# Kernel tuning notes

Measured on AMD Instinct MI355X. Metric: run time of the kernel, lower is better.

## Reference

```python
import jax, jax.numpy as jnp
import numpy as np

B, S, D_MODEL = 2, 2048, 2048
N_HEADS, N_KV_HEADS, D_HEAD = 32, 8, 64
INIT_STD = 0.02


def setup_inputs() -> dict:
    key = jax.random.key(0)
    k1, k2, k3, k4, k5 = jax.random.split(key, 5)
    return {
        "residual": jax.random.normal(k1, (B, S, D_MODEL), dtype=jnp.float32),
        "W_Q": jax.random.normal(k2, (N_HEADS, D_HEAD, D_MODEL), dtype=jnp.float32) * INIT_STD,
        "W_K": jax.random.normal(k3, (N_KV_HEADS, D_HEAD, D_MODEL), dtype=jnp.float32) * INIT_STD,
        "W_V": jax.random.normal(k4, (N_KV_HEADS, D_HEAD, D_MODEL), dtype=jnp.float32) * INIT_STD,
        "W_O": jax.random.normal(k5, (N_HEADS, D_HEAD, D_MODEL), dtype=jnp.float32) * INIT_STD,
    }


def reference(residual, W_Q, W_K, W_V, W_O):
    # QKV projections: residual [b,p,d] x W [n,h,d] -> [b,p,n,h]
    q = jnp.einsum('bpd,nhd->bpnh', residual, W_Q)
    k = jnp.einsum('bpd,nhd->bpnh', residual, W_K)
    v = jnp.einsum('bpd,nhd->bpnh', residual, W_V)

    # GQA: repeat_interleave kv heads up to n_heads
    rep = N_HEADS // N_KV_HEADS
    k = jnp.repeat(k, rep, axis=2)  # [b, p, n_heads, h]
    v = jnp.repeat(v, rep, axis=2)

    # scaled dot-product scores: [b, n, q, k]
    scores = jnp.einsum('bqnh,bknh->bnqk', q, k) / jnp.sqrt(jnp.float32(D_HEAD))

    # causal mask (seq_len == total_len, no cache)
    seq_len = residual.shape[1]
    causal = jnp.tril(jnp.ones((seq_len, seq_len), dtype=bool))
    scores = jnp.where(causal[None, None, :, :], scores, jnp.float32(-jnp.inf))

    pattern = jax.nn.softmax(scores, axis=-1)

    # weighted sum of values: [b, q, n, h]
    attn_out = jnp.einsum('bnqk,bknh->bqnh', pattern, v)

    # output projection: [b, q, d_model]
    out = jnp.einsum('bqnh,nhd->bqd', attn_out, W_O)
    return out
```

## Files before the change

kernel.cpp:

```cpp
#include <hip/hip_runtime.h>


typedef __attribute__((ext_vector_type(8))) short short8;
typedef __attribute__((ext_vector_type(4))) short short4v;
typedef __attribute__((ext_vector_type(4))) float f32x4;

__device__ __forceinline__ short f2bs(float f) {
  unsigned u = __float_as_uint(f);
  u = (u + 0x7fffu + ((u >> 16) & 1u)) >> 16;
  return (short)u;
}
__device__ __forceinline__ float bs2f(short s) {
  return __uint_as_float(((unsigned)(unsigned short)s) << 16);
}

__device__ __forceinline__ void async_ld16(const void* g, void* l) {
  __builtin_amdgcn_global_load_lds((__attribute__((address_space(1))) void*)(g),
                                   (__attribute__((address_space(3))) void*)(l),
                                   16, 0, 0);
}

#define BARRIER()                       \
  do {                                  \
    asm volatile("" ::: "memory");      \
    __builtin_amdgcn_s_barrier();       \
    asm volatile("" ::: "memory");      \
  } while (0)
#define LGKM0()                                          \
  do {                                                   \
    asm volatile("s_waitcnt lgkmcnt(0)" ::: "memory");   \
    __builtin_amdgcn_sched_barrier(0);                   \
  } while (0)
#define VMCNT(n) asm volatile("s_waitcnt vmcnt(" #n ")" ::: "memory")
#define MFMA16(a, b, c) \
  (c) = __builtin_amdgcn_mfma_f32_16x16x32_bf16((a), (b), (c), 0, 0, 0)

__device__ __forceinline__ short4v pk4bf16(float p0, float p1, float p2,
                                           float p3) {
  union {
    unsigned u[2];
    short4v s;
  } pk;
  asm("v_cvt_pk_bf16_f32 %0, %1, %2" : "=v"(pk.u[0]) : "v"(p0), "v"(p1));
  asm("v_cvt_pk_bf16_f32 %0, %1, %2" : "=v"(pk.u[1]) : "v"(p2), "v"(p3));
  return pk.s;
}

__device__ __forceinline__ int block_sniff_f32(const short* __restrict__ r,
                                               int* bad) {
  if (threadIdx.x == 0) *bad = 0;
  __syncthreads();
  int my = 0;
  for (int i = threadIdx.x; i < 512; i += blockDim.x) {
    float x = bs2f(r[i]);
    if (!(fabsf(x) < 100.0f)) my = 1;
  }
  if (my) atomicOr(bad, 1);
  __syncthreads();
  return *bad;
}

__global__ __launch_bounds__(256) void prep_kernel(
    const void* __restrict__ s0, const void* __restrict__ s1,
    const void* __restrict__ s2, const void* __restrict__ s3,
    short* __restrict__ d0, short* __restrict__ d1, short* __restrict__ d2,
    short* __restrict__ d3, const void* __restrict__ wo,
    short* __restrict__ wot) {
  __shared__ short tile[64][65];
  __shared__ int badsh;
  const int isf = block_sniff_f32((const short*)s0, &badsh);
  const int bid = blockIdx.x;
  if (bid < 7168) {
    long off = (long)bid * 256 + threadIdx.x;
    const void* src;
    short* dst;
    if (off < 1048576) {
      src = s0; dst = d0;
    } else if ((off -= 1048576) < 524288) {
      src = s1; dst = d1;
    } else if ((off -= 524288) < 131072) {
      src = s2; dst = d2;
    } else {
      off -= 131072; src = s3; dst = d3;
    }
    const long e = off * 8;
    short8 v;
    if (isf) {
      const float* f = (const float*)src + e;
      const f32x4 a = *(const f32x4*)(f);
      const f32x4 b = *(const f32x4*)(f + 4);
#pragma unroll
      for (int j = 0; j < 4; ++j) {
        v[j] = f2bs(a[j]);
        v[4 + j] = f2bs(b[j]);
      }
    } else {
      v = *(const short8*)((const short*)src + e);
    }
    *(short8*)(dst + e) = v;
  } else {
    const int tb = bid - 7168;
    const int bx = tb & 31, by = tb >> 5;
    const int tx = threadIdx.x & 63, ty = threadIdx.x >> 6;
#pragma unroll
    for (int i = 0; i < 16; ++i) {
      const int r = ty + i * 4;
      const size_t idx = (size_t)(by * 64 + r) * 2048 + bx * 64 + tx;
      tile[r][tx] =
          isf ? f2bs(((const float*)wo)[idx]) : ((const short*)wo)[idx];
    }
    __syncthreads();
#pragma unroll
    for (int i = 0; i < 16; ++i) {
      const int r = ty + i * 4;
      wot[(size_t)(bx * 64 + r) * 2048 + by * 64 + tx] = tile[tx][r];
    }
  }
}

__device__ __forceinline__ void gemm256(const short* __restrict__ A, int lda,
                                        const short* __restrict__ B, int ldb,
                                        void* __restrict__ C, int ldc,
                                        int rowBase, int colBase, int K,
                                        short* SM, int outF32, float cscale) {
  const int t = threadIdx.x;
  const int wave = t >> 6;
  const int lane = t & 63;
  const int quad = lane >> 4;
  const int m16 = lane & 15;
  const int wr = (wave >> 2) * 128;
  const int wc = (wave & 3) * 64;

  short* const As0 = SM;
  short* const As1 = SM + 16384;
  short* const Bs0 = SM + 32768;
  short* const Bs1 = SM + 49152;

  const int sr = t >> 3;
  const int sc8 = ((t & 7) ^ (sr & 7)) * 8;
  const short* aS = A + (size_t)(rowBase + sr) * lda + sc8;
  const short* bS = B + (size_t)(colBase + sr) * ldb + sc8;
  const int dOff = wave * 512;

#define STG_A(buf, rg, kt) \
  async_ld16(aS + (size_t)(rg) * lda + (kt) * 64, (buf) + (rg) * 64 + dOff)
#define STG_B(buf, rg, kt) \
  async_ld16(bS + (size_t)(rg) * ldb + (kt) * 64, (buf) + (rg) * 64 + dOff)
#define RD(buf, row0, kh)                          \
  (*(const short8*)((buf) + ((row0) + m16) * 64 +  \
                    ((((kh) * 4 + quad) ^ (m16 & 7)) * 8)))

  const int nT = K >> 6;
  STG_A(As0, 0, 0); STG_A(As0, 64, 0); STG_A(As0, 128, 0); STG_A(As0, 192, 0);
  STG_B(Bs0, 0, 0); STG_B(Bs0, 64, 0); STG_B(Bs0, 128, 0); STG_B(Bs0, 192, 0);
  if (nT > 1) {
    STG_A(As1, 0, 1); STG_A(As1, 64, 1); STG_A(As1, 128, 1); STG_A(As1, 192, 1);
  }

  f32x4 acc[8][4] = {};
  for (int tt = 0; tt < nT; ++tt) {
    short* const Ac = (tt & 1) ? As1 : As0;
    short* const Bc = (tt & 1) ? Bs1 : Bs0;
    short* const Bn = (tt & 1) ? Bs0 : Bs1;

    if (tt + 1 < nT) {
      VMCNT(4);
    } else {
      VMCNT(0);
    }
    BARRIER();

    short8 alo[4][2], blo[2][2];
#pragma unroll
    for (int i = 0; i < 4; ++i) {
      alo[i][0] = RD(Ac, wr + i * 16, 0);
      alo[i][1] = RD(Ac, wr + i * 16, 1);
    }
#pragma unroll
    for (int j = 0; j < 2; ++j) {
      blo[j][0] = RD(Bc, wc + j * 16, 0);
      blo[j][1] = RD(Bc, wc + j * 16, 1);
    }
    if (tt + 1 < nT) { STG_B(Bn, 0, tt + 1); STG_B(Bn, 64, tt + 1); }
    BARRIER();
    LGKM0();
    __builtin_amdgcn_s_setprio(1);
#pragma unroll
    for (int i = 0; i < 4; ++i)
#pragma unroll
      for (int j = 0; j < 2; ++j) {
        MFMA16(alo[i][0], blo[j][0], acc[i][j]);
        MFMA16(alo[i][1], blo[j][1], acc[i][j]);
      }
    __builtin_amdgcn_s_setprio(0);
    BARRIER();

    short8 bhi[2][2];
#pragma unroll
    for (int j = 0; j < 2; ++j) {
      bhi[j][0] = RD(Bc, wc + 32 + j * 16, 0);
      bhi[j][1] = RD(Bc, wc + 32 + j * 16, 1);
    }
    if (tt + 1 < nT) { STG_B(Bn, 128, tt + 1); STG_B(Bn, 192, tt + 1); }
    BARRIER();
    LGKM0();
    __builtin_amdgcn_s_setprio(1);
#pragma unroll
    for (int i = 0; i < 4; ++i)
#pragma unroll
      for (int j = 0; j < 2; ++j) {
        MFMA16(alo[i][0], bhi[j][0], acc[i][2 + j]);
        MFMA16(alo[i][1], bhi[j][1], acc[i][2 + j]);
      }
    __builtin_amdgcn_s_setprio(0);
    BARRIER();

    short8 ahi[4][2];
#pragma unroll
    for (int i = 0; i < 4; ++i) {
      ahi[i][0] = RD(Ac, wr + 64 + i * 16, 0);
      ahi[i][1] = RD(Ac, wr + 64 + i * 16, 1);
    }
    BARRIER();
    if (tt + 2 < nT) { STG_A(Ac, 0, tt + 2); STG_A(Ac, 64, tt + 2); }
    LGKM0();
    __builtin_amdgcn_s_setprio(1);
#pragma unroll
    for (int i = 0; i < 4; ++i)
#pragma unroll
      for (int j = 0; j < 2; ++j) {
        MFMA16(ahi[i][0], blo[j][0], acc[4 + i][j]);
        MFMA16(ahi[i][1], blo[j][1], acc[4 + i][j]);
      }
    __builtin_amdgcn_s_setprio(0);
    BARRIER();

    if (tt + 2 < nT) { STG_A(Ac, 128, tt + 2); STG_A(Ac, 192, tt + 2); }
    __builtin_amdgcn_s_setprio(1);
#pragma unroll
    for (int i = 0; i < 4; ++i)
#pragma unroll
      for (int j = 0; j < 2; ++j) {
        MFMA16(ahi[i][0], bhi[j][0], acc[4 + i][2 + j]);
        MFMA16(ahi[i][1], bhi[j][1], acc[4 + i][2 + j]);
      }
    __builtin_amdgcn_s_setprio(0);
  }

  float* const F = (float*)SM + wave * 4096;
#pragma unroll
  for (int h = 0; h < 2; ++h) {
    if (h) LGKM0();
#pragma unroll
    for (int i = 0; i < 4; ++i)
#pragma unroll
      for (int j = 0; j < 4; ++j)
#pragma unroll
        for (int r = 0; r < 4; ++r)
          F[(i * 16 + quad * 4 + r) * 64 + j * 16 + m16] =
              acc[h * 4 + i][j][r] * cscale;
    LGKM0();
#pragma unroll
    for (int p = 0; p < 16; ++p) {
      const int row = p * 4 + quad;
      const f32x4 vv = *(const f32x4*)(F + row * 64 + m16 * 4);
      const size_t gi =
          (size_t)(rowBase + wr + h * 64 + row) * ldc + colBase + wc + m16 * 4;
      if (outF32) {
        *(f32x4*)((float*)C + gi) = vv;
      } else {
        short4v s;
#pragma unroll
        for (int r = 0; r < 4; ++r) s[r] = f2bs(vv[r]);
        *(short4v*)((short*)C + gi) = s;
      }
    }
  }
#undef STG_A
#undef STG_B
#undef RD
}

__global__ __launch_bounds__(512, 2) void qkv_gemm_kernel(
    const short* __restrict__ R, const short* __restrict__ WQ,
    const short* __restrict__ WK, const short* __restrict__ WV,
    short* __restrict__ q, short* __restrict__ k, short* __restrict__ v) {
  __shared__ __align__(16) short SM[65536];
  const int lid = blockIdx.x;
  const int nl = (lid & 7) * 24 + (lid >> 3);
  const int ct = nl % 12;
  const int rt = nl / 12;
  const short* Bm;
  short* Cout;
  int colBase, ldc;
  float cs = 1.0f;
  if (ct < 8) {
    Bm = WQ; Cout = q; colBase = ct * 256; ldc = 2048;
    cs = 0.125f * 1.44269504088896340736f;
  } else if (ct < 10) {
    Bm = WK; Cout = k; colBase = (ct - 8) * 256; ldc = 512;
  } else {
    Bm = WV; Cout = v; colBase = (ct - 10) * 256; ldc = 512;
  }
  gemm256(R, 2048, Bm, 2048, Cout, ldc, rt * 256, colBase, 2048, SM, 0, cs);
}

__global__ __launch_bounds__(512, 2) void out_gemm_kernel(
    const short* __restrict__ A, const short* __restrict__ Bt,
    void* __restrict__ C, const short* __restrict__ sniffsrc) {
  __shared__ __align__(16) short SM[65536];
  const int outF32 = block_sniff_f32(sniffsrc, (int*)SM);
  const int lid = blockIdx.x;
  const int nl = (lid & 7) * 16 + (lid >> 3);
  const int ct = nl & 7;
  const int rt = nl >> 3;
  gemm256(A, 2048, Bt, 2048, C, 2048, rt * 256, ct * 256, 2048, SM, outF32,
          1.0f);
}

__global__ __launch_bounds__(256) void vt_kernel(const short* __restrict__ v,
                                                 short* __restrict__ vt) {
  __shared__ short tile[64][65];
  const int hb = blockIdx.x * 64, pb = blockIdx.y * 64, b = blockIdx.z;
  const int tx = threadIdx.x & 63, ty = threadIdx.x >> 6;
#pragma unroll
  for (int i = 0; i < 16; ++i) {
    const int r = ty + i * 4;
    tile[r][tx] = v[((size_t)(b * 2048 + pb + r)) * 512 + hb + tx];
  }
  __syncthreads();
#pragma unroll
  for (int i = 0; i < 16; ++i) {
    const int r = ty + i * 4;
    vt[((size_t)(b * 512 + hb + r)) * 2048 + pb + tx] = tile[tx][r];
  }
}

__global__ __launch_bounds__(256, 3) void attn_kernel(
    const short* __restrict__ qbuf, const short* __restrict__ kbuf,
    const short* __restrict__ vtb, short* __restrict__ obuf) {
  __shared__ __align__(16) short Ks[2][64 * 64];
  __shared__ __align__(16) short Vs[2][64 * 64];
  __shared__ __align__(16) short Pb[4][32 * 64];

  const int b = blockIdx.x >> 3;
  const int kv = blockIdx.x & 7;
  const int qc = 63 - blockIdx.y;
  const int t = threadIdx.x;
  const int wave = t >> 6;
  const int hd = kv * 4 + wave;
  const int lane = t & 63;
  const int quad = lane >> 4;
  const int col = lane & 15;
  const int rb0 = qc * 32;

  short8 qf[2][2];
#pragma unroll
  for (int nt = 0; nt < 2; ++nt) {
    const int qr = rb0 + nt * 16 + col;
    const short* qp = qbuf + ((size_t)(b * 2048 + qr)) * 2048 + hd * 64 + quad * 8;
    qf[nt][0] = *(const short8*)(qp);
    qf[nt][1] = *(const short8*)(qp + 32);
  }

  float lloc[2] = {0.f, 0.f};
  f32x4 oacc[2][4] = {};

  short* P = &Pb[wave][0];
  const int swz = 4 * (col & 3);

  const int sRow = t >> 3;
  const int sPos = t & 7;
  const int r1 = sRow + 32;
  const short* kRow0 = kbuf + ((size_t)(b * 2048 + sRow)) * 512 + kv * 64 +
                       ((sPos ^ (sRow & 7)) * 8);
  const short* kRow1 = kbuf + ((size_t)(b * 2048 + r1)) * 512 + kv * 64 +
                       ((sPos ^ (r1 & 7)) * 8);
  const short* vRow0 = vtb + ((size_t)(b * 512 + kv * 64 + sRow)) * 2048 +
                       ((sPos ^ (sRow & 7)) * 8);
  const short* vRow1 = vtb + ((size_t)(b * 512 + kv * 64 + r1)) * 2048 +
                       ((sPos ^ (r1 & 7)) * 8);

  const int nkt = (qc >> 1) + 1;

  async_ld16(kRow0, &Ks[0][wave * 512]);
  async_ld16(kRow1, &Ks[0][2048 + wave * 512]);
  async_ld16(vRow0, &Vs[0][wave * 512]);
  async_ld16(vRow1, &Vs[0][2048 + wave * 512]);

  for (int kt = 0; kt < nkt; ++kt) {
    __syncthreads();
    if (kt + 1 < nkt) {
      const int nb = (kt + 1) & 1;
      const size_t ko = (size_t)(kt + 1) * 64 * 512;
      const int vo = (kt + 1) * 64;
      async_ld16(kRow0 + ko, &Ks[nb][wave * 512]);
      async_ld16(kRow1 + ko, &Ks[nb][2048 + wave * 512]);
      async_ld16(vRow0 + vo, &Vs[nb][wave * 512]);
      async_ld16(vRow1 + vo, &Vs[nb][2048 + wave * 512]);
    }
    const int ktb = kt * 64;
    const short* ks = &Ks[kt & 1][0];
    const short* vs = &Vs[kt & 1][0];

    short8 kf[4][2];
#pragma unroll
    for (int mt = 0; mt < 4; ++mt) {
      const int krow = mt * 16 + col;
      kf[mt][0] = *(const short8*)(ks + krow * 64 + ((quad ^ (col & 7)) * 8));
      kf[mt][1] = *(const short8*)(ks + krow * 64 + (((4 + quad) ^ (col & 7)) * 8));
    }

#pragma unroll
    for (int nt = 0; nt < 2; ++nt) {
      const int rb = rb0 + nt * 16;

      f32x4 st[4];
#pragma unroll
      for (int mt = 0; mt < 4; ++mt) {
        f32x4 z = {0.f, 0.f, 0.f, 0.f};
        z = __builtin_amdgcn_mfma_f32_16x16x32_bf16(kf[mt][0], qf[nt][0], z, 0, 0, 0);
        z = __builtin_amdgcn_mfma_f32_16x16x32_bf16(kf[mt][1], qf[nt][1], z, 0, 0, 0);
        st[mt] = z;
      }

      if (ktb + 63 > rb) {
        const int qrow = rb + col;
#pragma unroll
        for (int mt = 0; mt < 4; ++mt)
#pragma unroll
          for (int r = 0; r < 4; ++r)
            if (ktb + mt * 16 + quad * 4 + r > qrow) st[mt][r] = -1.0e30f;
      }

      float rs = 0.f;
#pragma unroll
      for (int mt = 0; mt < 4; ++mt) {
        const float p0 = exp2f(st[mt][0]);
        const float p1 = exp2f(st[mt][1]);
        const float p2 = exp2f(st[mt][2]);
        const float p3 = exp2f(st[mt][3]);
        rs += (p0 + p1) + (p2 + p3);
        *(short4v*)(P + (nt * 16 + col) * 64 + (quad + 4 * (mt ^ (col & 3))) * 4) =
            pk4bf16(p0, p1, p2, p3);
      }
      {
        const float a = __shfl_xor(rs, 16, 64);
        const float d = __shfl_xor(rs, 32, 64);
        const float e = __shfl_xor(rs, 48, 64);
        rs = (rs + a) + (d + e);
      }
      lloc[nt] += rs;
    }

    asm volatile("s_waitcnt lgkmcnt(0)" ::: "memory");

    short8 pf[2][2];
#pragma unroll
    for (int nt = 0; nt < 2; ++nt) {
      const int base = (nt * 16 + col) * 64;
      pf[nt][0] = *(const short8*)(P + base + ((2 * quad) ^ swz) * 4);
      pf[nt][1] = *(const short8*)(P + base + ((8 + 2 * quad) ^ swz) * 4);
    }

#pragma unroll
    for (int ct = 0; ct < 4; ++ct) {
      const int h = ct * 16 + col;
      const short8 va = *(const short8*)(vs + h * 64 + ((quad ^ (col & 7)) * 8));
      const short8 vb = *(const short8*)(vs + h * 64 + (((4 + quad) ^ (col & 7)) * 8));
#pragma unroll
      for (int nt = 0; nt < 2; ++nt) {
        oacc[nt][ct] = __builtin_amdgcn_mfma_f32_16x16x32_bf16(
            va, pf[nt][0], oacc[nt][ct], 0, 0, 0);
        oacc[nt][ct] = __builtin_amdgcn_mfma_f32_16x16x32_bf16(
            vb, pf[nt][1], oacc[nt][ct], 0, 0, 0);
      }
    }
  }

  const float inv0 = 1.0f / lloc[0];
  const float inv1 = 1.0f / lloc[1];
#pragma unroll
  for (int nt = 0; nt < 2; ++nt) {
    const float inv = nt ? inv1 : inv0;
#pragma unroll
    for (int ct = 0; ct < 4; ++ct) {
      *(short4v*)(P + (nt * 16 + col) * 64 + ct * 16 + quad * 4) =
          pk4bf16(oacc[nt][ct][0] * inv, oacc[nt][ct][1] * inv,
                  oacc[nt][ct][2] * inv, oacc[nt][ct][3] * inv);
    }
  }
  asm volatile("s_waitcnt lgkmcnt(0)" ::: "memory");
#pragma unroll
  for (int p = 0; p < 4; ++p) {
    const int qlocal = (lane >> 3) + 8 * p;
    const short8 row = *(const short8*)(P + qlocal * 64 + (lane & 7) * 8);
    *(short8*)(obuf + ((size_t)(b * 2048 + rb0 + qlocal)) * 2048 + hd * 64 +
               (lane & 7) * 8) = row;
  }
}

extern "C" void kernel_launch(void* const* d_in, const int* in_sizes, int n_in,
                              void* d_out, int out_size, void* d_ws,
                              size_t ws_size, hipStream_t stream) {
  char* ws = (char*)d_ws;
  short* rbuf = (short*)(ws + 256);
  short* wqb = rbuf + 8388608;
  short* wkb = wqb + 4194304;
  short* wvb = wkb + 1048576;
  short* kbuf = wvb + 1048576;
  short* vbuf = kbuf + 2097152;
  short* abuf = vbuf + 2097152;
  short* wot = abuf + 8388608;
  short* vtb = wqb;
  short* qbuf = (short*)d_out;

  hipLaunchKernelGGL(prep_kernel, dim3(8192), dim3(256), 0, stream,
                     d_in[0], d_in[1], d_in[2], d_in[3], rbuf, wqb, wkb, wvb,
                     d_in[4], wot);
  hipLaunchKernelGGL(qkv_gemm_kernel, dim3(192), dim3(512), 0, stream,
                     rbuf, wqb, wkb, wvb, qbuf, kbuf, vbuf);
  hipLaunchKernelGGL(vt_kernel, dim3(8, 32, 2), dim3(256), 0, stream,
                     vbuf, vtb);
  hipLaunchKernelGGL(attn_kernel, dim3(16, 64), dim3(256), 0, stream,
                     qbuf, kbuf, vtb, abuf);
  hipLaunchKernelGGL(out_gemm_kernel, dim3(128), dim3(512), 0, stream,
                     abuf, wot, (void*)d_out, (const short*)d_in[0]);
}
```

Measured before the change: 302.3 us.

## Use 256x128 tiles for output GEMM and MFMA-based softmax row sums

Adds a 256x128-tile GEMM variant for the output projection and launches 256 blocks instead of 128, which should fill more compute units on the MI355X. In the attention kernel, the per-row probability sums are now computed with an MFMA against a vector of bf16 ones instead of scalar adds plus cross-lane shuffles. The MFMA sum uses the bf16-rounded probabilities, so the normaliser matches the values actually fed to the PV product. The smaller tile lowers operand reuse per block and adds some extra global traffic.

```diff
diff --git a/kernel.cpp b/kernel.cpp
--- a/kernel.cpp
+++ b/kernel.cpp
@@ -281,6 +281,125 @@
 #undef RD
 }
 
+__device__ __forceinline__ void gemm256x128(const short* __restrict__ A,
+                                            int lda,
+                                            const short* __restrict__ B,
+                                            int ldb, void* __restrict__ C,
+                                            int ldc, int rowBase, int colBase,
+                                            int K, short* SM, int outF32) {
+  const int t = threadIdx.x;
+  const int wave = t >> 6;
+  const int lane = t & 63;
+  const int quad = lane >> 4;
+  const int m16 = lane & 15;
+  const int wr = (wave >> 1) * 64;
+  const int wc = (wave & 1) * 64;
+
+  short* const As0 = SM;
+  short* const As1 = SM + 16384;
+  short* const Bs0 = SM + 32768;
+  short* const Bs1 = SM + 40960;
+
+  const int sr = t >> 3;
+  const int sc8 = ((t & 7) ^ (sr & 7)) * 8;
+  const short* aS = A + (size_t)(rowBase + sr) * lda + sc8;
+  const short* bS = B + (size_t)(colBase + sr) * ldb + sc8;
+  const int dOff = wave * 512;
+
+#define STG_A(buf, rg, kt) \
+  async_ld16(aS + (size_t)(rg) * lda + (kt) * 64, (buf) + (rg) * 64 + dOff)
+#define STG_B(buf, rg, kt) \
+  async_ld16(bS + (size_t)(rg) * ldb + (kt) * 64, (buf) + (rg) * 64 + dOff)
+#define RD(buf, row0, kh)                          \
+  (*(const short8*)((buf) + ((row0) + m16) * 64 +  \
+                    ((((kh) * 4 + quad) ^ (m16 & 7)) * 8)))
+
+  const int nT = K >> 6;
+  STG_A(As0, 0, 0); STG_A(As0, 64, 0); STG_A(As0, 128, 0); STG_A(As0, 192, 0);
+  STG_B(Bs0, 0, 0); STG_B(Bs0, 64, 0);
+  if (nT > 1) {
+    STG_A(As1, 0, 1); STG_A(As1, 64, 1); STG_A(As1, 128, 1); STG_A(As1, 192, 1);
+  }
+
+  f32x4 acc[4][4] = {};
+  for (int tt = 0; tt < nT; ++tt) {
+    short* const Ac = (tt & 1) ? As1 : As0;
+    short* const Bc = (tt & 1) ? Bs1 : Bs0;
+    short* const Bn = (tt & 1) ? Bs0 : Bs1;
+
+    if (tt + 1 < nT) {
+      VMCNT(4);
+    } else {
+      VMCNT(0);
+    }
+    BARRIER();
+
+    short8 a0[4], b0[4];
+#pragma unroll
+    for (int i = 0; i < 4; ++i) a0[i] = RD(Ac, wr + i * 16, 0);
+#pragma unroll
+    for (int j = 0; j < 4; ++j) b0[j] = RD(Bc, wc + j * 16, 0);
+    if (tt + 1 < nT) { STG_B(Bn, 0, tt + 1); STG_B(Bn, 64, tt + 1); }
+    BARRIER();
+    LGKM0();
+    __builtin_amdgcn_s_setprio(1);
+#pragma unroll
+    for (int i = 0; i < 4; ++i)
+#pragma unroll
+      for (int j = 0; j < 4; ++j) MFMA16(a0[i], b0[j], acc[i][j]);
+    __builtin_amdgcn_s_setprio(0);
+    BARRIER();
+
+    short8 a1[4], b1[4];
+#pragma unroll
+    for (int i = 0; i < 4; ++i) a1[i] = RD(Ac, wr + i * 16, 1);
+#pragma unroll
+    for (int j = 0; j < 4; ++j) b1[j] = RD(Bc, wc + j * 16, 1);
+    BARRIER();
+    LGKM0();
+    __builtin_amdgcn_s_setprio(1);
+#pragma unroll
+    for (int i = 0; i < 4; ++i)
+#pragma unroll
+      for (int j = 0; j < 4; ++j) MFMA16(a1[i], b1[j], acc[i][j]);
+    __builtin_amdgcn_s_setprio(0);
+    BARRIER();
+
+    if (tt + 2 < nT) {
+      STG_A(Ac, 0, tt + 2); STG_A(Ac, 64, tt + 2);
+      STG_A(Ac, 128, tt + 2); STG_A(Ac, 192, tt + 2);
+    }
+  }
+
+  float* const F = (float*)SM + wave * 4096;
+#pragma unroll
+  for (int i = 0; i < 4; ++i)
+#pragma unroll
+    for (int j = 0; j < 4; ++j)
+#pragma unroll
+      for (int r = 0; r < 4; ++r)
+        F[(i * 16 + quad * 4 + r) * 64 + j * 16 + m16] = acc[i][j][r];
+  LGKM0();
+#pragma unroll
+  for (int p = 0; p < 16; ++p) {
+    const int row = p * 4 + quad;
+    const f32x4 vv = *(const f32x4*)(F + row * 64 + m16 * 4);
+    const size_t gi =
+        (size_t)(rowBase + wr + row) * ldc + colBase + wc + m16 * 4;
+    if (outF32) {
+      *(f32x4*)((float*)C + gi) = vv;
+    } else {
+      short4v s;
+#pragma unroll
+      for (int r = 0; r < 4; ++r) s[r] = f2bs(vv[r]);
+      *(short4v*)((short*)C + gi) = s;
+    }
+  }
+#undef STG_A
+#undef STG_B
+#undef RD
+}
+
 __global__ __launch_bounds__(512, 2) void qkv_gemm_kernel(
     const short* __restrict__ R, const short* __restrict__ WQ,
     const short* __restrict__ WK, const short* __restrict__ WV,
@@ -311,11 +430,11 @@
   __shared__ __align__(16) short SM[65536];
   const int outF32 = block_sniff_f32(sniffsrc, (int*)SM);
   const int lid = blockIdx.x;
-  const int nl = (lid & 7) * 16 + (lid >> 3);
-  const int ct = nl & 7;
-  const int rt = nl >> 3;
-  gemm256(A, 2048, Bt, 2048, C, 2048, rt * 256, ct * 256, 2048, SM, outF32,
-          1.0f);
+  const int nl = (lid & 7) * 32 + (lid >> 3);
+  const int ct = nl & 15;
+  const int rt = nl >> 4;
+  gemm256x128(A, 2048, Bt, 2048, C, 2048, rt * 256, ct * 128, 2048, SM,
+              outF32);
 }
 
 __global__ __launch_bounds__(256) void vt_kernel(const short* __restrict__ v,
@@ -363,8 +482,12 @@
     qf[nt][1] = *(const short8*)(qp + 32);
   }
 
-  float lloc[2] = {0.f, 0.f};
+  short8 ones;
+#pragma unroll
+  for (int i = 0; i < 8; ++i) ones[i] = (short)0x3F80;
+
   f32x4 oacc[2][4] = {};
+  f32x4 sacc[2] = {};
 
   short* P = &Pb[wave][0];
   const int swz = 4 * (col & 3);
@@ -433,24 +556,15 @@
             if (ktb + mt * 16 + quad * 4 + r > qrow) st[mt][r] = -1.0e30f;
       }
 
-      float rs = 0.f;
 #pragma unroll
       for (int mt = 0; mt < 4; ++mt) {
         const float p0 = exp2f(st[mt][0]);
         const float p1 = exp2f(st[mt][1]);
         const float p2 = exp2f(st[mt][2]);
         const float p3 = exp2f(st[mt][3]);
-        rs += (p0 + p1) + (p2 + p3);
         *(short4v*)(P + (nt * 16 + col) * 64 + (quad + 4 * (mt ^ (col & 3))) * 4) =
             pk4bf16(p0, p1, p2, p3);
       }
-      {
-        const float a = __shfl_xor(rs, 16, 64);
-        const float d = __shfl_xor(rs, 32, 64);
-        const float e = __shfl_xor(rs, 48, 64);
-        rs = (rs + a) + (d + e);
-      }
-      lloc[nt] += rs;
     }
 
     asm volatile("s_waitcnt lgkmcnt(0)" ::: "memory");
@@ -461,6 +575,14 @@
       const int base = (nt * 16 + col) * 64;
       pf[nt][0] = *(const short8*)(P + base + ((2 * quad) ^ swz) * 4);
       pf[nt][1] = *(const short8*)(P + base + ((8 + 2 * quad) ^ swz) * 4);
+    }
+
+#pragma unroll
+    for (int nt = 0; nt < 2; ++nt) {
+      sacc[nt] = __builtin_amdgcn_mfma_f32_16x16x32_bf16(ones, pf[nt][0],
+                                                         sacc[nt], 0, 0, 0);
+      sacc[nt] = __builtin_amdgcn_mfma_f32_16x16x32_bf16(ones, pf[nt][1],
+                                                         sacc[nt], 0, 0, 0);
     }
 
 #pragma unroll
@@ -478,8 +600,8 @@
     }
   }
 
-  const float inv0 = 1.0f / lloc[0];
-  const float inv1 = 1.0f / lloc[1];
+  const float inv0 = 1.0f / sacc[0][0];
+  const float inv1 = 1.0f / sacc[1][0];
 #pragma unroll
   for (int nt = 0; nt < 2; ++nt) {
     const float inv = nt ? inv1 : inv0;
@@ -524,6 +646,6 @@
                      vbuf, vtb);
   hipLaunchKernelGGL(attn_kernel, dim3(16, 64), dim3(256), 0, stream,
                      qbuf, kbuf, vtb, abuf);
-  hipLaunchKernelGGL(out_gemm_kernel, dim3(128), dim3(512), 0, stream,
+  hipLaunchKernelGGL(out_gemm_kernel, dim3(256), dim3(512), 0, stream,
                      abuf, wot, (void*)d_out, (const short*)d_in[0]);
 }
```

Measured after the change: 280.8 us. 7.1% less time.
